# Kernel tuning notes

Hardware: AMD Instinct MI355X
Metric: run time of the kernel (lower is better)

## Reference

```python
import jax, jax.numpy as jnp
import numpy as np

B, DIN, H, DOUT, NC = 1024, 343, 512, 311, 4


def cubic(y0, y1, y2, y3, mu):
    # Catmull-Rom cubic interpolation (matches PFNN.cubic)
    return ((-0.5 * y0 + 1.5 * y1 - 1.5 * y2 + 0.5 * y3) * mu * mu * mu
            + (y0 - 2.5 * y1 + 2.0 * y2 - 0.5 * y3) * mu * mu
            + (-0.5 * y0 + 0.5 * y2) * mu + y1)


def setup_inputs() -> dict:
    key = jax.random.key(0)
    ks = jax.random.split(key, 7)
    s = 0.05
    x = jax.random.uniform(ks[0], (B, DIN), dtype=jnp.float32)  # phase = x[:, -1] in [0,1)
    W0 = jax.random.normal(ks[1], (NC, H, DIN - 1), dtype=jnp.float32) * s
    W1 = jax.random.normal(ks[2], (NC, H, H), dtype=jnp.float32) * s
    W2 = jax.random.normal(ks[3], (NC, DOUT, H), dtype=jnp.float32) * s
    b0 = jax.random.normal(ks[4], (NC, H), dtype=jnp.float32) * s
    b1 = jax.random.normal(ks[5], (NC, H), dtype=jnp.float32) * s
    b2 = jax.random.normal(ks[6], (NC, DOUT), dtype=jnp.float32) * s
    return {"x": x, "W0": W0, "W1": W1, "W2": W2, "b0": b0, "b1": b1, "b2": b2}


def reference(x, W0, W1, W2, b0, b1, b2):
    nc = W0.shape[0]
    phase = x[:, -1]                       # [B]
    pscale = nc * phase
    mu = jnp.mod(pscale, 1.0)              # [B]
    k1 = jnp.mod(pscale.astype(jnp.int32), nc)
    k0 = jnp.mod(k1 - 1, nc)
    k2 = jnp.mod(k1 + 1, nc)
    k3 = jnp.mod(k1 + 2, nc)
    muW = mu[:, None, None]
    mub = mu[:, None]

    def interp(P, m):
        return cubic(P[k0], P[k1], P[k2], P[k3], m)

    W0i = interp(W0, muW)  # [B, 512, DIN-1]
    W1i = interp(W1, muW)  # [B, 512, 512]
    W2i = interp(W2, muW)  # [B, DOUT, 512]
    b0i = interp(b0, mub)
    b1i = interp(b1, mub)
    b2i = interp(b2, mub)

    h0 = x[:, :-1]                                              # [B, DIN-1]
    h1 = jax.nn.elu(jnp.einsum('boi,bi->bo', W0i, h0) + b0i)    # [B, 512]
    h2 = jax.nn.elu(jnp.einsum('boi,bi->bo', W1i, h1) + b1i)    # [B, 512]
    h3 = jnp.einsum('boi,bi->bo', W2i, h2) + b2i                # [B, DOUT]
    return h3
```

## Files before the change

kernel.cpp:

```cpp
#include <hip/hip_runtime.h>
#include <math.h>

typedef short bf16x8 __attribute__((ext_vector_type(8)));
typedef float f32x16 __attribute__((ext_vector_type(16)));

__device__ __forceinline__ unsigned short f2bf(float f) {
    union { float f; unsigned u; } x; x.f = f;
    unsigned r = x.u + 0x7FFFu + ((x.u >> 16) & 1u);
    return (unsigned short)(r >> 16);
}

__device__ __forceinline__ bf16x8 conv8(const float* __restrict__ W,
                                        const float* __restrict__ bias,
                                        int row, int Kreal, int k0) {
    bf16x8 r;
    #pragma unroll
    for (int j = 0; j < 8; ++j) {
        int k = k0 + j;
        float v = (k < Kreal) ? W[(size_t)row * Kreal + k]
                              : ((k == Kreal) ? bias[row] : 0.f);
        r[j] = (short)f2bf(v);
    }
    return r;
}

__global__ void __launch_bounds__(256) phaseA_kernel(
    const float* __restrict__ x,
    const float* __restrict__ W0, const float* __restrict__ W1, const float* __restrict__ W2,
    const float* __restrict__ bias0, const float* __restrict__ bias1, const float* __restrict__ bias2,
    float* __restrict__ coef, unsigned short* __restrict__ xf,
    unsigned short* __restrict__ H1f, unsigned short* __restrict__ H2f,
    unsigned short* __restrict__ Wf0, unsigned short* __restrict__ Wf1, unsigned short* __restrict__ Wf2)
{
    const unsigned gtid = blockIdx.x * 256u + threadIdx.x;
    const unsigned gsz  = gridDim.x * 256u;

    for (unsigned b = gtid; b < 1024u; b += gsz) {
        float phase = x[b * 343u + 342u];
        float ps = 4.0f * phase;
        int k1 = (int)ps;
        float mu = ps - (float)k1;
        k1 &= 3;
        float mu2 = mu * mu, mu3 = mu2 * mu;
        float c0 = -0.5f * mu3 +        mu2 - 0.5f * mu;
        float c1 =  1.5f * mu3 - 2.5f * mu2 + 1.0f;
        float c2 = -1.5f * mu3 + 2.0f * mu2 + 0.5f * mu;
        float c3 =  0.5f * mu3 - 0.5f * mu2;
        float cc[4];
        cc[(k1 + 3) & 3] = c0;
        cc[k1]           = c1;
        cc[(k1 + 1) & 3] = c2;
        cc[(k1 + 2) & 3] = c3;
        *(float4*)(coef + b * 4) = make_float4(cc[0], cc[1], cc[2], cc[3]);
    }

    for (unsigned c = gtid; c < 32u * 24u * 64u; c += gsz) {
        unsigned lane = c & 63u, r = c >> 6;
        unsigned ks = r % 24u, bt = r / 24u;
        int b  = (int)(bt * 32u + (lane & 31u));
        int k0 = (int)(ks * 16u + (lane >> 5) * 8u);
        bf16x8 v;
        #pragma unroll
        for (int j = 0; j < 8; ++j) {
            int k = k0 + j;
            unsigned short s;
            if (k < 342)       s = f2bf(x[(size_t)b * 343 + k]);
            else if (k == 342) s = 0x3F80;
            else               s = 0;
            v[j] = (short)s;
        }
        *(bf16x8*)(xf + (size_t)c * 8) = v;
    }

    for (unsigned c = gtid; c < 32u * 4u * 64u; c += gsz) {
        unsigned lane = c & 63u, r = c >> 6;
        unsigned kk = r & 3u, bt = r >> 2;
        size_t off = ((size_t)(bt * 36u + 32u + kk) * 64u + lane) * 8u;
        bf16x8 v;
        #pragma unroll
        for (int j = 0; j < 8; ++j)
            v[j] = (short)((kk == 0u && (lane >> 5) == 0u && j == 0) ? 0x3F80 : 0);
        *(bf16x8*)(H1f + off) = v;
        *(bf16x8*)(H2f + off) = v;
    }

    constexpr unsigned C0 = 4u * 16 * 24 * 64;
    constexpr unsigned C1 = 4u * 16 * 36 * 64;
    constexpr unsigned C2 = 4u * 10 * 36 * 64;
    for (unsigned c = gtid; c < C0 + C1 + C2; c += gsz) {
        bf16x8 v;
        unsigned short* dst;
        if (c < C0) {
            unsigned lane = c & 63u, r = c >> 6, ks = r % 24u, t = r / 24u;
            int o  = (int)((t & 15u) * 32u + (lane & 31u));
            int k0 = (int)(ks * 16u + (lane >> 5) * 8u);
            v = conv8(W0, bias0, (int)(t >> 4) * 512 + o, 342, k0);
            dst = Wf0 + (size_t)c * 8;
        } else if (c < C0 + C1) {
            unsigned cc = c - C0;
            unsigned lane = cc & 63u, r = cc >> 6, ks = r % 36u, t = r / 36u;
            int o  = (int)((t & 15u) * 32u + (lane & 31u));
            int k0 = (int)(ks * 16u + (lane >> 5) * 8u);
            v = conv8(W1, bias1, (int)(t >> 4) * 512 + o, 512, k0);
            dst = Wf1 + (size_t)cc * 8;
        } else {
            unsigned cc = c - C0 - C1;
            unsigned lane = cc & 63u, r = cc >> 6, ks = r % 36u, t = r / 36u;
            unsigned ot = t % 10u, n = t / 10u;
            int o  = (int)(ot * 32u + (lane & 31u));
            int k0 = (int)(ks * 16u + (lane >> 5) * 8u);
            if (o < 311) {
                v = conv8(W2, bias2, (int)n * 311 + o, 512, k0);
            } else {
                #pragma unroll
                for (int j = 0; j < 8; ++j) v[j] = 0;
            }
            dst = Wf2 + (size_t)cc * 8;
        }
        *(bf16x8*)dst = v;
    }
}

template<bool ELU, bool OUT_BF16, int KP, int OPAD>
__device__ __forceinline__ void layer_phase(
    const unsigned short* __restrict__ Wf,
    const unsigned short* __restrict__ Hf,
    const float* __restrict__ coef,
    unsigned short* __restrict__ HoutF,
    float* __restrict__ outF, int Oreal,
    float* red, int bid, int tid, int gdim)
{
    constexpr int NOT = OPAD / 32, NKS = KP / 16, KSQ = NKS / 4;
    const int lane = tid & 63, w = tid >> 6;
    const int m = lane & 31, h = lane >> 5;
    const size_t nstr = (size_t)NOT * NKS * 512;

    for (int t = bid; t < NOT * 32; t += gdim) {
        const int ot = t >> 5, bt = t & 31;
        const unsigned short* wbase = Wf + ((size_t)ot * NKS + w * KSQ) * 512 + (size_t)lane * 8;
        const unsigned short* bbase = Hf + ((size_t)bt * NKS + w * KSQ) * 512 + (size_t)lane * 8;

        f32x16 acc0 = {}, acc1 = {}, acc2 = {}, acc3 = {};
        #pragma unroll
        for (int s = 0; s < KSQ; ++s) {
            bf16x8 bfr = *(const bf16x8*)(bbase + (size_t)s * 512);
            bf16x8 a0 = *(const bf16x8*)(wbase + (size_t)s * 512);
            bf16x8 a1 = *(const bf16x8*)(wbase + nstr + (size_t)s * 512);
            bf16x8 a2 = *(const bf16x8*)(wbase + 2 * nstr + (size_t)s * 512);
            bf16x8 a3 = *(const bf16x8*)(wbase + 3 * nstr + (size_t)s * 512);
            acc0 = __builtin_amdgcn_mfma_f32_32x32x16_bf16(a0, bfr, acc0, 0, 0, 0);
            acc1 = __builtin_amdgcn_mfma_f32_32x32x16_bf16(a1, bfr, acc1, 0, 0, 0);
            acc2 = __builtin_amdgcn_mfma_f32_32x32x16_bf16(a2, bfr, acc2, 0, 0, 0);
            acc3 = __builtin_amdgcn_mfma_f32_32x32x16_bf16(a3, bfr, acc3, 0, 0, 0);
        }

        const int b = bt * 32 + m;
        float4 cf = *(const float4*)(coef + b * 4);
        float sv[16];
        #pragma unroll
        for (int r = 0; r < 16; ++r)
            sv[r] = cf.x * acc0[r] + cf.y * acc1[r] + cf.z * acc2[r] + cf.w * acc3[r];

        __syncthreads();
        if (w > 0) {
            #pragma unroll
            for (int g = 0; g < 4; ++g)
                #pragma unroll
                for (int j = 0; j < 4; ++j) {
                    int row = 8 * g + 4 * h + j;
                    red[(w - 1) * 1024 + row * 32 + m] = sv[g * 4 + j];
                }
        }
        __syncthreads();
        if (w == 0) {
            #pragma unroll
            for (int g = 0; g < 4; ++g) {
                float vv[4];
                #pragma unroll
                for (int j = 0; j < 4; ++j) {
                    int row = 8 * g + 4 * h + j;
                    float v = sv[g * 4 + j] + red[row * 32 + m]
                            + red[1024 + row * 32 + m] + red[2048 + row * 32 + m];
                    if (ELU) v = (v > 0.f) ? v : expm1f(v);
                    vv[j] = v;
                }
                if (OUT_BF16) {
                    size_t off = (((size_t)bt * 36 + ot * 2 + (g >> 1)) * 64
                                  + (g & 1) * 32 + m) * 8 + 4 * h;
                    ushort4 pk;
                    pk.x = f2bf(vv[0]); pk.y = f2bf(vv[1]); pk.z = f2bf(vv[2]); pk.w = f2bf(vv[3]);
                    *(ushort4*)(HoutF + off) = pk;
                } else {
                    int orow = ot * 32 + 8 * g + 4 * h;
                    #pragma unroll
                    for (int j = 0; j < 4; ++j)
                        if (orow + j < Oreal) outF[(size_t)b * Oreal + orow + j] = vv[j];
                }
            }
        }
    }
}

__global__ void __launch_bounds__(256, 2) layer0_kernel(
    const unsigned short* __restrict__ Wf0, const unsigned short* __restrict__ xf,
    const float* __restrict__ coef, unsigned short* __restrict__ H1f)
{
    __shared__ float red[3 * 1024];
    layer_phase<true, true, 384, 512>(Wf0, xf, coef, H1f, nullptr, 512,
                                      red, blockIdx.x, threadIdx.x, gridDim.x);
}
__global__ void __launch_bounds__(256, 2) layer1_kernel(
    const unsigned short* __restrict__ Wf1, const unsigned short* __restrict__ H1f,
    const float* __restrict__ coef, unsigned short* __restrict__ H2f)
{
    __shared__ float red[3 * 1024];
    layer_phase<true, true, 576, 512>(Wf1, H1f, coef, H2f, nullptr, 512,
                                      red, blockIdx.x, threadIdx.x, gridDim.x);
}
__global__ void __launch_bounds__(256, 2) layer2_kernel(
    const unsigned short* __restrict__ Wf2, const unsigned short* __restrict__ H2f,
    const float* __restrict__ coef, float* __restrict__ outF)
{
    __shared__ float red[3 * 1024];
    layer_phase<false, false, 576, 320>(Wf2, H2f, coef, nullptr, outF, 311,
                                        red, blockIdx.x, threadIdx.x, gridDim.x);
}

extern "C" void kernel_launch(void* const* d_in, const int* in_sizes, int n_in,
                              void* d_out, int out_size, void* d_ws, size_t ws_size,
                              hipStream_t stream) {
    (void)in_sizes; (void)n_in; (void)out_size; (void)ws_size;
    const float* x  = (const float*)d_in[0];
    const float* W0 = (const float*)d_in[1];
    const float* W1 = (const float*)d_in[2];
    const float* W2 = (const float*)d_in[3];
    const float* b0 = (const float*)d_in[4];
    const float* b1 = (const float*)d_in[5];
    const float* b2 = (const float*)d_in[6];
    float* out = (float*)d_out;

    char* wsb = (char*)d_ws;
    float*          coef = (float*)(wsb + 0);
    unsigned short* xf   = (unsigned short*)(wsb + 16384);
    unsigned short* H1f  = (unsigned short*)(wsb + 802816);
    unsigned short* H2f  = (unsigned short*)(wsb + 1982464);
    unsigned short* Wf0  = (unsigned short*)(wsb + 3162112);
    unsigned short* Wf1  = (unsigned short*)(wsb + 4734976);
    unsigned short* Wf2  = (unsigned short*)(wsb + 7094272);

    phaseA_kernel<<<dim3(512), dim3(256), 0, stream>>>(
        x, W0, W1, W2, b0, b1, b2, coef, xf, H1f, H2f, Wf0, Wf1, Wf2);
    layer0_kernel<<<dim3(512), dim3(256), 0, stream>>>(Wf0, xf,  coef, H1f);
    layer1_kernel<<<dim3(512), dim3(256), 0, stream>>>(Wf1, H1f, coef, H2f);
    layer2_kernel<<<dim3(320), dim3(256), 0, stream>>>(Wf2, H2f, coef, out);
}
```

Measured before the change: 100.7 us.

## Transpose weights through LDS tiles and double-buffer MFMA operand loads

The preprocessing kernel now assigns one block per 32-row tile and stages coalesced fp32 row reads through shared memory before writing the bf16 MFMA fragment layout. Previously each thread gathered 8 strided elements per row. The layer kernels drop the grid-stride loop and prefetch the next chunk of A/B fragments into registers while MFMAs run on the current chunk. The cross-wave reduction now spreads the epilogue over all four waves instead of wave 0 alone. The trade-off is more register pressure from the double buffers and fewer blocks (200) in the preprocessing kernel.

```diff
diff --git a/kernel.cpp b/kernel.cpp
--- a/kernel.cpp
+++ b/kernel.cpp
@@ -10,18 +10,45 @@
     return (unsigned short)(r >> 16);
 }
 
-__device__ __forceinline__ bf16x8 conv8(const float* __restrict__ W,
-                                        const float* __restrict__ bias,
-                                        int row, int Kreal, int k0) {
-    bf16x8 r;
-    #pragma unroll
-    for (int j = 0; j < 8; ++j) {
-        int k = k0 + j;
-        float v = (k < Kreal) ? W[(size_t)row * Kreal + k]
-                              : ((k == Kreal) ? bias[row] : 0.f);
-        r[j] = (short)f2bf(v);
-    }
-    return r;
+template<int NKS_T>
+__device__ void transpose_tile(const float* __restrict__ W, const float* __restrict__ bias,
+                               int rowbase, int rowlimit, int Kreal, int ldsrc,
+                               unsigned short* __restrict__ dst, float* s, int tid)
+{
+    constexpr int NCHK = NKS_T / 4;
+    const int r = tid >> 3, l = tid & 7;
+    const int ks_l = tid >> 6, lane = tid & 63;
+    const int m = lane & 31, h = lane >> 5;
+    for (int kc = 0; kc < NCHK; ++kc) {
+        {
+            int kb = kc * 64 + l * 8;
+            const bool rv = r < rowlimit;
+            const float* src = W + (size_t)(rowbase + r) * ldsrc + kb;
+            float v[8];
+            if (rv && kb + 7 < Kreal) {
+                #pragma unroll
+                for (int i = 0; i < 8; ++i) v[i] = src[i];
+            } else {
+                #pragma unroll
+                for (int i = 0; i < 8; ++i) {
+                    int k = kb + i;
+                    v[i] = (rv && k < Kreal) ? src[i]
+                         : ((rv && k == Kreal) ? (bias ? bias[rowbase + r] : 1.0f) : 0.f);
+                }
+            }
+            #pragma unroll
+            for (int i = 0; i < 8; ++i) s[r * 66 + l * 8 + i] = v[i];
+        }
+        __syncthreads();
+        {
+            bf16x8 pk;
+            #pragma unroll
+            for (int j = 0; j < 8; ++j)
+                pk[j] = (short)f2bf(s[m * 66 + ks_l * 16 + h * 8 + j]);
+            *(bf16x8*)(dst + ((size_t)(kc * 4 + ks_l) * 64 + lane) * 8) = pk;
+        }
+        __syncthreads();
+    }
 }
 
 __global__ void __launch_bounds__(256) phaseA_kernel(
@@ -32,92 +59,55 @@
     unsigned short* __restrict__ H1f, unsigned short* __restrict__ H2f,
     unsigned short* __restrict__ Wf0, unsigned short* __restrict__ Wf1, unsigned short* __restrict__ Wf2)
 {
-    const unsigned gtid = blockIdx.x * 256u + threadIdx.x;
-    const unsigned gsz  = gridDim.x * 256u;
-
-    for (unsigned b = gtid; b < 1024u; b += gsz) {
-        float phase = x[b * 343u + 342u];
-        float ps = 4.0f * phase;
-        int k1 = (int)ps;
-        float mu = ps - (float)k1;
-        k1 &= 3;
-        float mu2 = mu * mu, mu3 = mu2 * mu;
-        float c0 = -0.5f * mu3 +        mu2 - 0.5f * mu;
-        float c1 =  1.5f * mu3 - 2.5f * mu2 + 1.0f;
-        float c2 = -1.5f * mu3 + 2.0f * mu2 + 0.5f * mu;
-        float c3 =  0.5f * mu3 - 0.5f * mu2;
-        float cc[4];
-        cc[(k1 + 3) & 3] = c0;
-        cc[k1]           = c1;
-        cc[(k1 + 1) & 3] = c2;
-        cc[(k1 + 2) & 3] = c3;
-        *(float4*)(coef + b * 4) = make_float4(cc[0], cc[1], cc[2], cc[3]);
-    }
-
-    for (unsigned c = gtid; c < 32u * 24u * 64u; c += gsz) {
-        unsigned lane = c & 63u, r = c >> 6;
-        unsigned ks = r % 24u, bt = r / 24u;
-        int b  = (int)(bt * 32u + (lane & 31u));
-        int k0 = (int)(ks * 16u + (lane >> 5) * 8u);
-        bf16x8 v;
-        #pragma unroll
-        for (int j = 0; j < 8; ++j) {
-            int k = k0 + j;
-            unsigned short s;
-            if (k < 342)       s = f2bf(x[(size_t)b * 343 + k]);
-            else if (k == 342) s = 0x3F80;
-            else               s = 0;
-            v[j] = (short)s;
-        }
-        *(bf16x8*)(xf + (size_t)c * 8) = v;
-    }
-
-    for (unsigned c = gtid; c < 32u * 4u * 64u; c += gsz) {
-        unsigned lane = c & 63u, r = c >> 6;
-        unsigned kk = r & 3u, bt = r >> 2;
-        size_t off = ((size_t)(bt * 36u + 32u + kk) * 64u + lane) * 8u;
-        bf16x8 v;
-        #pragma unroll
-        for (int j = 0; j < 8; ++j)
-            v[j] = (short)((kk == 0u && (lane >> 5) == 0u && j == 0) ? 0x3F80 : 0);
-        *(bf16x8*)(H1f + off) = v;
-        *(bf16x8*)(H2f + off) = v;
-    }
-
-    constexpr unsigned C0 = 4u * 16 * 24 * 64;
-    constexpr unsigned C1 = 4u * 16 * 36 * 64;
-    constexpr unsigned C2 = 4u * 10 * 36 * 64;
-    for (unsigned c = gtid; c < C0 + C1 + C2; c += gsz) {
-        bf16x8 v;
-        unsigned short* dst;
-        if (c < C0) {
-            unsigned lane = c & 63u, r = c >> 6, ks = r % 24u, t = r / 24u;
-            int o  = (int)((t & 15u) * 32u + (lane & 31u));
-            int k0 = (int)(ks * 16u + (lane >> 5) * 8u);
-            v = conv8(W0, bias0, (int)(t >> 4) * 512 + o, 342, k0);
-            dst = Wf0 + (size_t)c * 8;
-        } else if (c < C0 + C1) {
-            unsigned cc = c - C0;
-            unsigned lane = cc & 63u, r = cc >> 6, ks = r % 36u, t = r / 36u;
-            int o  = (int)((t & 15u) * 32u + (lane & 31u));
-            int k0 = (int)(ks * 16u + (lane >> 5) * 8u);
-            v = conv8(W1, bias1, (int)(t >> 4) * 512 + o, 512, k0);
-            dst = Wf1 + (size_t)cc * 8;
-        } else {
-            unsigned cc = c - C0 - C1;
-            unsigned lane = cc & 63u, r = cc >> 6, ks = r % 36u, t = r / 36u;
-            unsigned ot = t % 10u, n = t / 10u;
-            int o  = (int)(ot * 32u + (lane & 31u));
-            int k0 = (int)(ks * 16u + (lane >> 5) * 8u);
-            if (o < 311) {
-                v = conv8(W2, bias2, (int)n * 311 + o, 512, k0);
-            } else {
-                #pragma unroll
-                for (int j = 0; j < 8; ++j) v[j] = 0;
-            }
-            dst = Wf2 + (size_t)cc * 8;
-        }
-        *(bf16x8*)dst = v;
+    __shared__ float s[32 * 66];
+    const int bid = blockIdx.x, tid = threadIdx.x;
+
+    if (bid < 32) {
+        const int bt = bid;
+        if (tid < 32) {
+            int b = bt * 32 + tid;
+            float phase = x[(size_t)b * 343 + 342];
+            float ps = 4.0f * phase;
+            int k1 = (int)ps;
+            float mu = ps - (float)k1;
+            k1 &= 3;
+            float mu2 = mu * mu, mu3 = mu2 * mu;
+            float c0 = -0.5f * mu3 +        mu2 - 0.5f * mu;
+            float c1 =  1.5f * mu3 - 2.5f * mu2 + 1.0f;
+            float c2 = -1.5f * mu3 + 2.0f * mu2 + 0.5f * mu;
+            float c3 =  0.5f * mu3 - 0.5f * mu2;
+            float cc[4];
+            cc[(k1 + 3) & 3] = c0;
+            cc[k1]           = c1;
+            cc[(k1 + 1) & 3] = c2;
+            cc[(k1 + 2) & 3] = c3;
+            *(float4*)(coef + b * 4) = make_float4(cc[0], cc[1], cc[2], cc[3]);
+        }
+        {
+            int kk = tid >> 6, lane = tid & 63;
+            size_t off = ((size_t)(bt * 36 + 32 + kk) * 64 + lane) * 8;
+            bf16x8 v;
+            #pragma unroll
+            for (int j = 0; j < 8; ++j)
+                v[j] = (short)((kk == 0 && (lane >> 5) == 0 && j == 0) ? 0x3F80 : 0);
+            *(bf16x8*)(H1f + off) = v;
+            *(bf16x8*)(H2f + off) = v;
+        }
+        transpose_tile<24>(x, nullptr, bt * 32, 32, 342, 343,
+                           xf + (size_t)bt * 24 * 512, s, tid);
+    } else if (bid < 96) {
+        int idx = bid - 32, n = idx >> 4, ot = idx & 15;
+        transpose_tile<24>(W0, bias0, n * 512 + ot * 32, 32, 342, 342,
+                           Wf0 + (size_t)(n * 16 + ot) * 24 * 512, s, tid);
+    } else if (bid < 160) {
+        int idx = bid - 96, n = idx >> 4, ot = idx & 15;
+        transpose_tile<36>(W1, bias1, n * 512 + ot * 32, 32, 512, 512,
+                           Wf1 + (size_t)(n * 16 + ot) * 36 * 512, s, tid);
+    } else {
+        int idx = bid - 160, n = idx / 10, ot = idx % 10;
+        int rl = 311 - ot * 32; if (rl > 32) rl = 32;
+        transpose_tile<36>(W2, bias2, n * 311 + ot * 32, rl, 512, 512,
+                           Wf2 + (size_t)(n * 10 + ot) * 36 * 512, s, tid);
     }
 }
 
@@ -128,75 +118,83 @@
     const float* __restrict__ coef,
     unsigned short* __restrict__ HoutF,
     float* __restrict__ outF, int Oreal,
-    float* red, int bid, int tid, int gdim)
+    float* red, int bid, int tid)
 {
     constexpr int NOT = OPAD / 32, NKS = KP / 16, KSQ = NKS / 4;
+    constexpr int CH = 3, NC2 = KSQ / CH;
     const int lane = tid & 63, w = tid >> 6;
     const int m = lane & 31, h = lane >> 5;
     const size_t nstr = (size_t)NOT * NKS * 512;
 
-    for (int t = bid; t < NOT * 32; t += gdim) {
-        const int ot = t >> 5, bt = t & 31;
-        const unsigned short* wbase = Wf + ((size_t)ot * NKS + w * KSQ) * 512 + (size_t)lane * 8;
-        const unsigned short* bbase = Hf + ((size_t)bt * NKS + w * KSQ) * 512 + (size_t)lane * 8;
-
-        f32x16 acc0 = {}, acc1 = {}, acc2 = {}, acc3 = {};
-        #pragma unroll
-        for (int s = 0; s < KSQ; ++s) {
-            bf16x8 bfr = *(const bf16x8*)(bbase + (size_t)s * 512);
-            bf16x8 a0 = *(const bf16x8*)(wbase + (size_t)s * 512);
-            bf16x8 a1 = *(const bf16x8*)(wbase + nstr + (size_t)s * 512);
-            bf16x8 a2 = *(const bf16x8*)(wbase + 2 * nstr + (size_t)s * 512);
-            bf16x8 a3 = *(const bf16x8*)(wbase + 3 * nstr + (size_t)s * 512);
-            acc0 = __builtin_amdgcn_mfma_f32_32x32x16_bf16(a0, bfr, acc0, 0, 0, 0);
-            acc1 = __builtin_amdgcn_mfma_f32_32x32x16_bf16(a1, bfr, acc1, 0, 0, 0);
-            acc2 = __builtin_amdgcn_mfma_f32_32x32x16_bf16(a2, bfr, acc2, 0, 0, 0);
-            acc3 = __builtin_amdgcn_mfma_f32_32x32x16_bf16(a3, bfr, acc3, 0, 0, 0);
-        }
-
-        const int b = bt * 32 + m;
-        float4 cf = *(const float4*)(coef + b * 4);
-        float sv[16];
-        #pragma unroll
-        for (int r = 0; r < 16; ++r)
-            sv[r] = cf.x * acc0[r] + cf.y * acc1[r] + cf.z * acc2[r] + cf.w * acc3[r];
-
-        __syncthreads();
-        if (w > 0) {
-            #pragma unroll
-            for (int g = 0; g < 4; ++g)
+    const int ot = bid >> 5, bt = bid & 31;
+    const unsigned short* wbase = Wf + ((size_t)ot * NKS + w * KSQ) * 512 + (size_t)lane * 8;
+    const unsigned short* bbase = Hf + ((size_t)bt * NKS + w * KSQ) * 512 + (size_t)lane * 8;
+
+    f32x16 acc0 = {}, acc1 = {}, acc2 = {}, acc3 = {};
+    bf16x8 Ab[2][CH][4], Bb[2][CH];
+
+    #pragma unroll
+    for (int sI = 0; sI < CH; ++sI) {
+        Bb[0][sI] = *(const bf16x8*)(bbase + (size_t)sI * 512);
+        #pragma unroll
+        for (int n = 0; n < 4; ++n)
+            Ab[0][sI][n] = *(const bf16x8*)(wbase + (size_t)n * nstr + (size_t)sI * 512);
+    }
+    #pragma unroll
+    for (int c = 0; c < NC2; ++c) {
+        const int cur = c & 1;
+        if (c + 1 < NC2) {
+            const int nxt = cur ^ 1;
+            #pragma unroll
+            for (int sI = 0; sI < CH; ++sI) {
+                int st = (c + 1) * CH + sI;
+                Bb[nxt][sI] = *(const bf16x8*)(bbase + (size_t)st * 512);
                 #pragma unroll
-                for (int j = 0; j < 4; ++j) {
-                    int row = 8 * g + 4 * h + j;
-                    red[(w - 1) * 1024 + row * 32 + m] = sv[g * 4 + j];
-                }
-        }
-        __syncthreads();
-        if (w == 0) {
-            #pragma unroll
-            for (int g = 0; g < 4; ++g) {
-                float vv[4];
-                #pragma unroll
-                for (int j = 0; j < 4; ++j) {
-                    int row = 8 * g + 4 * h + j;
-                    float v = sv[g * 4 + j] + red[row * 32 + m]
-                            + red[1024 + row * 32 + m] + red[2048 + row * 32 + m];
-                    if (ELU) v = (v > 0.f) ? v : expm1f(v);
-                    vv[j] = v;
-                }
-                if (OUT_BF16) {
-                    size_t off = (((size_t)bt * 36 + ot * 2 + (g >> 1)) * 64
-                                  + (g & 1) * 32 + m) * 8 + 4 * h;
-                    ushort4 pk;
-                    pk.x = f2bf(vv[0]); pk.y = f2bf(vv[1]); pk.z = f2bf(vv[2]); pk.w = f2bf(vv[3]);
-                    *(ushort4*)(HoutF + off) = pk;
-                } else {
-                    int orow = ot * 32 + 8 * g + 4 * h;
-                    #pragma unroll
-                    for (int j = 0; j < 4; ++j)
-                        if (orow + j < Oreal) outF[(size_t)b * Oreal + orow + j] = vv[j];
-                }
+                for (int n = 0; n < 4; ++n)
+                    Ab[nxt][sI][n] = *(const bf16x8*)(wbase + (size_t)n * nstr + (size_t)st * 512);
             }
+        }
+        #pragma unroll
+        for (int sI = 0; sI < CH; ++sI) {
+            acc0 = __builtin_amdgcn_mfma_f32_32x32x16_bf16(Ab[cur][sI][0], Bb[cur][sI], acc0, 0, 0, 0);
+            acc1 = __builtin_amdgcn_mfma_f32_32x32x16_bf16(Ab[cur][sI][1], Bb[cur][sI], acc1, 0, 0, 0);
+            acc2 = __builtin_amdgcn_mfma_f32_32x32x16_bf16(Ab[cur][sI][2], Bb[cur][sI], acc2, 0, 0, 0);
+            acc3 = __builtin_amdgcn_mfma_f32_32x32x16_bf16(Ab[cur][sI][3], Bb[cur][sI], acc3, 0, 0, 0);
+        }
+    }
+
+    const int b = bt * 32 + m;
+    float4 cf = *(const float4*)(coef + b * 4);
+    #pragma unroll
+    for (int g = 0; g < 4; ++g)
+        #pragma unroll
+        for (int j = 0; j < 4; ++j) {
+            int rI = g * 4 + j;
+            float v = cf.x * acc0[rI] + cf.y * acc1[rI] + cf.z * acc2[rI] + cf.w * acc3[rI];
+            red[w * 1024 + (8 * g + 4 * h + j) * 32 + m] = v;
+        }
+    __syncthreads();
+    {
+        float vv[4];
+        #pragma unroll
+        for (int j = 0; j < 4; ++j) {
+            int row = 8 * w + 4 * h + j;
+            float v = red[row * 32 + m] + red[1024 + row * 32 + m]
+                    + red[2048 + row * 32 + m] + red[3072 + row * 32 + m];
+            if (ELU) v = (v > 0.f) ? v : expm1f(v);
+            vv[j] = v;
+        }
+        if (OUT_BF16) {
+            size_t off = (((size_t)bt * 36 + ot * 2 + (w >> 1)) * 64
+                          + (w & 1) * 32 + m) * 8 + 4 * h;
+            ushort4 pk;
+            pk.x = f2bf(vv[0]); pk.y = f2bf(vv[1]); pk.z = f2bf(vv[2]); pk.w = f2bf(vv[3]);
+            *(ushort4*)(HoutF + off) = pk;
+        } else {
+            int orow = ot * 32 + 8 * w + 4 * h;
+            #pragma unroll
+            for (int j = 0; j < 4; ++j)
+                if (orow + j < Oreal) outF[(size_t)b * Oreal + orow + j] = vv[j];
         }
     }
 }
@@ -205,25 +203,25 @@
     const unsigned short* __restrict__ Wf0, const unsigned short* __restrict__ xf,
     const float* __restrict__ coef, unsigned short* __restrict__ H1f)
 {
-    __shared__ float red[3 * 1024];
+    __shared__ float red[4 * 1024];
     layer_phase<true, true, 384, 512>(Wf0, xf, coef, H1f, nullptr, 512,
-                                      red, blockIdx.x, threadIdx.x, gridDim.x);
+                                      red, blockIdx.x, threadIdx.x);
 }
 __global__ void __launch_bounds__(256, 2) layer1_kernel(
     const unsigned short* __restrict__ Wf1, const unsigned short* __restrict__ H1f,
     const float* __restrict__ coef, unsigned short* __restrict__ H2f)
 {
-    __shared__ float red[3 * 1024];
+    __shared__ float red[4 * 1024];
     layer_phase<true, true, 576, 512>(Wf1, H1f, coef, H2f, nullptr, 512,
-                                      red, blockIdx.x, threadIdx.x, gridDim.x);
+                                      red, blockIdx.x, threadIdx.x);
 }
 __global__ void __launch_bounds__(256, 2) layer2_kernel(
     const unsigned short* __restrict__ Wf2, const unsigned short* __restrict__ H2f,
     const float* __restrict__ coef, float* __restrict__ outF)
 {
-    __shared__ float red[3 * 1024];
+    __shared__ float red[4 * 1024];
     layer_phase<false, false, 576, 320>(Wf2, H2f, coef, nullptr, outF, 311,
-                                        red, blockIdx.x, threadIdx.x, gridDim.x);
+                                        red, blockIdx.x, threadIdx.x);
 }
 
 extern "C" void kernel_launch(void* const* d_in, const int* in_sizes, int n_in,
@@ -248,7 +246,7 @@
     unsigned short* Wf1  = (unsigned short*)(wsb + 4734976);
     unsigned short* Wf2  = (unsigned short*)(wsb + 7094272);
 
-    phaseA_kernel<<<dim3(512), dim3(256), 0, stream>>>(
+    phaseA_kernel<<<dim3(200), dim3(256), 0, stream>>>(
         x, W0, W1, W2, b0, b1, b2, coef, xf, H1f, H2f, Wf0, Wf1, Wf2);
     layer0_kernel<<<dim3(512), dim3(256), 0, stream>>>(Wf0, xf,  coef, H1f);
     layer1_kernel<<<dim3(512), dim3(256), 0, stream>>>(Wf1, H1f, coef, H2f);
```

Measured after the change: 94.91 us. -5.7%, faster.
